# Kernel tuning notes

Hardware: AMD Instinct MI355X
Metric: run time of the kernel (lower is better)

## Reference

```python
import jax, jax.numpy as jnp
import numpy as np

EMBED_DIM = 256
NUM_HEADS = 8
NUM_QUERIES = 448
TEMPERATURE = 10000.0
SCALE = 100.0
EPS = 1e-5
B, N = 1, 512
NUM_CLASSES = 91


def box_rel_encoding(src_boxes, tgt_boxes, eps=EPS):
    # boxes: [B, N, 4] as (cx, cy, w, h)
    xy1, wh1 = src_boxes[..., :2], src_boxes[..., 2:]
    xy2, wh2 = tgt_boxes[..., :2], tgt_boxes[..., 2:]
    delta_xy = jnp.abs(xy1[..., :, None, :] - xy2[..., None, :, :])          # [B,N,N,2]
    delta_xy = jnp.log(delta_xy / (wh1[..., :, None, :] + eps) + 1.0)
    delta_wh = jnp.log((wh1[..., :, None, :] + eps) / (wh2[..., None, :, :] + eps))
    return jnp.concatenate([delta_xy, delta_wh], axis=-1)                    # [B,N,N,4]


def get_sine_pos_embed(pos, num_pos_feats, temperature=TEMPERATURE, scale=SCALE):
    # pos: [..., C]; returns [..., C * num_pos_feats]; exchange_xy=False
    dim_t = jnp.arange(num_pos_feats, dtype=pos.dtype)
    dim_t = temperature ** (2.0 * jnp.floor(dim_t / 2.0) / num_pos_feats)
    x = pos[..., None] * scale / dim_t                                        # [...,C,F]
    emb = jnp.stack([jnp.sin(x[..., 0::2]), jnp.cos(x[..., 1::2])], axis=-1)  # [...,C,F/2,2]
    emb = emb.reshape(x.shape)                                                # [...,C,F]
    return emb.reshape(pos.shape[:-1] + (pos.shape[-1] * num_pos_feats,))


def setup_inputs() -> dict:
    key = jax.random.key(0)
    ks = jax.random.split(key, 9)
    s = 0.02
    return {
        "src_boxes": jax.random.uniform(ks[0], (B, N, 4), jnp.float32, 0.05, 0.95),
        "pred_logits": jax.random.normal(ks[1], (B, N, NUM_CLASSES), jnp.float32),
        "rank_emb": jax.random.normal(ks[2], (NUM_QUERIES, EMBED_DIM), jnp.float32) * s,
        "pre_W": jax.random.normal(ks[3], (EMBED_DIM, EMBED_DIM), jnp.float32) * s,
        "pre_b": jax.random.normal(ks[4], (EMBED_DIM,), jnp.float32) * s,
        "post_W": jax.random.normal(ks[5], (EMBED_DIM, 2 * EMBED_DIM), jnp.float32) * s,
        "post_b": jax.random.normal(ks[6], (EMBED_DIM,), jnp.float32) * s,
        "attn_W": jax.random.normal(ks[7], (NUM_HEADS, EMBED_DIM), jnp.float32) * s,
        "attn_b": jax.random.normal(ks[8], (NUM_HEADS,), jnp.float32) * s,
        "layer_idx": 2,
    }


def reference(src_boxes, pred_logits, rank_emb, pre_W, pre_b, post_W, post_b, attn_W, attn_b, layer_idx):
    num_denoising = N - NUM_QUERIES
    # --- no-grad block: pairwise box relation + rank-ordered gather reorder ---
    base = box_rel_encoding(src_boxes, src_boxes)                            # [B,N,N,4]
    scores = jnp.max(jax.nn.sigmoid(pred_logits[:, num_denoising:]), axis=-1)  # [B,Q]
    order = jnp.argsort(-scores, axis=1)                                      # descending  [B,Q]
    rank_indices = jnp.broadcast_to(jnp.arange(N, dtype=order.dtype), (B, N))
    rank_indices = rank_indices.at[:, num_denoising:].set(order + num_denoising)
    nr = base[:, num_denoising:, num_denoising:]                              # [B,Q,Q,4]
    nr = jnp.take_along_axis(nr, order[:, :, None, None], axis=1)
    nr = jnp.take_along_axis(nr, order[:, None, :, None], axis=2)
    base = base.at[:, num_denoising:, num_denoising:].set(nr)
    base = jax.lax.stop_gradient(base)
    # --- sine positional embedding of relation: [B,N,N,EMBED_DIM] ---
    pos = get_sine_pos_embed(base, EMBED_DIM // 4)
    # --- rank-aware relation: embedding -> pre linear -> pairwise sum ---
    normal_rank = rank_emb @ pre_W.T + pre_b                                  # [Q,E]
    rank_rel = jnp.zeros((B, N, EMBED_DIM), src_boxes.dtype)
    rank_rel = rank_rel.at[:, num_denoising:].set(normal_rank[None])
    rank_rel = rank_rel[:, :, None, :] + rank_rel[:, None, :, :]              # [B,N,N,E]
    relation = jnp.concatenate([pos, rank_rel], axis=-1)                      # [B,N,N,2E]
    relation = relation @ post_W.T + post_b                                   # [B,N,N,E]
    attn = jax.nn.relu(relation @ attn_W.T + attn_b)                          # [B,N,N,H]
    attn = jnp.transpose(attn, (0, 3, 1, 2))                                  # [B,H,N,N]
    return attn, rank_indices
```

## Files before the change

kernel.cpp:

```cpp
#include <hip/hip_runtime.h>
#include <hip/hip_bf16.h>
#include <math.h>

#define NN 512
#define NQ 448
#define ND 64
#define NC 91
#define ED 256
#define NH 8

typedef __attribute__((ext_vector_type(8))) short bf16x8;
typedef __attribute__((ext_vector_type(4))) float f32x4;

struct FreqArg { float fr[32]; };

__device__ int   g_perm[NN];
__device__ float g_WK[2048];
__device__ float g_c0[NH];
__device__ float g_afull[NN * NH];
__device__ float g_part[64 * 512];
__device__ float g_pu[64 * ED];
__device__ float g_pb2a[64];
__device__ float g_scores[NQ];
__device__ __align__(16) unsigned short g_WB[8 * 64 * 8];

__device__ inline unsigned short f2bfbits(float x) {
    __hip_bfloat16 h = __float2bfloat16(x);
    union { __hip_bfloat16 b; unsigned short u; } cv; cv.b = h; return cv.u;
}

__global__ __launch_bounds__(512) void precomp_fold(const float* __restrict__ logits,
                                                    const float* __restrict__ attn_W,
                                                    const float* __restrict__ attn_b,
                                                    const float* __restrict__ post_W,
                                                    const float* __restrict__ post_b) {
    int bid = blockIdx.x;
    int t = threadIdx.x;
    if (bid < 64) {
        int h = bid >> 3, cc = bid & 7;
        __shared__ float sAW[32];
        if (t < 32) sAW[t] = attn_W[h * ED + cc * 32 + t];
        __syncthreads();
        float m = 0.f;
        const float* pw = post_W + (size_t)(cc * 32) * 512 + t;
#pragma unroll
        for (int ci = 0; ci < 32; ++ci) m = fmaf(sAW[ci], pw[(size_t)ci * 512], m);
        g_part[(size_t)bid * 512 + t] = m;
    } else if (bid < 72) {
        int W = (bid - 64) * 8 + (t >> 6);
        int lane = t & 63;
        for (int qi = 0; qi < 7; ++qi) {
            int q = W * 7 + qi;
            const float* row = logits + (size_t)(ND + q) * NC;
            float m = (lane < NC) ? row[lane] : -INFINITY;
            int c2 = lane + 64;
            if (c2 < NC) m = fmaxf(m, row[c2]);
            for (int off = 32; off > 0; off >>= 1) m = fmaxf(m, __shfl_down(m, off, 64));
            if (lane == 0) g_scores[q] = m;
        }
    } else {
        int h = t >> 6, lane = t & 63;
        float v = 0.f;
#pragma unroll
        for (int k = 0; k < 4; ++k) {
            int c = lane + 64 * k;
            v = fmaf(attn_W[h * ED + c], post_b[c], v);
        }
        for (int off = 32; off > 0; off >>= 1) v += __shfl_down(v, off, 64);
        if (lane == 0) g_c0[h] = attn_b[h] + v;
    }
}

__global__ __launch_bounds__(256) void precomp_u(const float* __restrict__ pre_W,
                                                 const float* __restrict__ pre_b,
                                                 float* __restrict__ out2) {
    int bid = blockIdx.x;
    int t = threadIdx.x;
    if (bid < 64) {
        int h = bid >> 3, dc = bid & 7;
        __shared__ float sw[32];
        if (t < 32) {
            int d = dc * 32 + t;
            float s = 0.f;
#pragma unroll
            for (int cc = 0; cc < 8; ++cc) s += g_part[(size_t)(h * 8 + cc) * 512 + 256 + d];
            sw[t] = s;
        } else if (t < 64) {
            int dl = t - 32;
            int d = dc * 32 + dl;
            float s = 0.f;
#pragma unroll
            for (int cc = 0; cc < 8; ++cc) s += g_part[(size_t)(h * 8 + cc) * 512 + d];
            int f = d >> 6, rem = d & 63, k = rem >> 1, r = rem & 1;
            g_WK[(k * 4 + f) * 16 + h * 2 + r] = s;
        }
        __syncthreads();
        if (t == 0) {
            float b = 0.f;
            for (int dl = 0; dl < 32; ++dl) b = fmaf(sw[dl], pre_b[dc * 32 + dl], b);
            g_pb2a[h * 8 + dc] = b;
        }
        float acc = 0.f;
        const float* pw = pre_W + (size_t)(dc * 32) * ED + t;
#pragma unroll
        for (int dl = 0; dl < 32; ++dl) acc = fmaf(sw[dl], pw[(size_t)dl * ED], acc);
        g_pu[(size_t)(h * 8 + dc) * ED + t] = acc;
    } else {
        __shared__ float sc[NQ];
        for (int v = t; v < NQ; v += 256) sc[v] = g_scores[v];
        __syncthreads();
        int q1 = t, q2 = t + 256;
        float s1 = sc[q1];
        float s2 = (q2 < NQ) ? sc[q2] : 0.f;
        int r1 = 0, r2 = 0;
        for (int j = 0; j < NQ; ++j) {
            float sj = sc[j];
            r1 += ((sj > s1) || (sj == s1 && j < q1)) ? 1 : 0;
            r2 += ((sj > s2) || (sj == s2 && j < q2)) ? 1 : 0;
        }
        g_perm[ND + r1] = ND + q1;
        out2[ND + r1] = (float)(ND + q1);
        if (q2 < NQ) {
            g_perm[ND + r2] = ND + q2;
            out2[ND + r2] = (float)(ND + q2);
        }
        if (t < ND) {
            g_perm[t] = t;
            out2[t] = (float)t;
            for (int h = 0; h < NH; ++h) g_afull[t * NH + h] = 0.f;
        }
    }
}

#define PAD 260
__global__ __launch_bounds__(256) void precomp_afull(const float* __restrict__ rank_emb) {
    int t = threadIdx.x;
    if (blockIdx.x == 14) {
        for (int v = t; v < 4096; v += 256) {
            int s = v >> 9;
            int lane = (v >> 3) & 63;
            int ii = v & 7;
            int g = lane >> 4, hh = lane & 15;
            int k = s * 4 + (ii >> 1), r = ii & 1;
            float w = (hh < NH) ? g_WK[((k * 4 + g) << 4) + hh * 2 + r] : 0.f;
            g_WB[v] = f2bfbits(w);
        }
        return;
    }
    __shared__ float sU[NH][PAD];
    __shared__ float sR[32][PAD];
    __shared__ float sb2a[NH];
    int q0 = blockIdx.x * 32;
    for (int v = t; v < NH * ED; v += 256) {
        int h = v >> 8, c = v & 255;
        float s = 0.f;
#pragma unroll
        for (int dc = 0; dc < 8; ++dc) s += g_pu[(size_t)(h * 8 + dc) * ED + c];
        sU[h][c] = s;
    }
    if (t < NH) {
        float s = 0.f;
#pragma unroll
        for (int dc = 0; dc < 8; ++dc) s += g_pb2a[t * 8 + dc];
        sb2a[t] = s;
    }
    for (int v = t; v < 32 * ED; v += 256)
        sR[v >> 8][v & 255] = rank_emb[(size_t)(q0 + (v >> 8)) * ED + (v & 255)];
    __syncthreads();
    int qloc = t >> 3, h = t & 7;
    float acc = sb2a[h];
    for (int c = 0; c < ED; ++c) acc = fmaf(sR[qloc][c], sU[h][c], acc);
    g_afull[(size_t)(ND + q0 + qloc) * NH + h] = acc;
}

__global__ __launch_bounds__(256) void relation_main(const float* __restrict__ boxes,
                                                     FreqArg fa,
                                                     float* __restrict__ out) {
    __shared__ bf16x8 sWB[8][64];
    int t = threadIdx.x;
    ((uint4*)sWB)[t]       = ((const uint4*)g_WB)[t];
    ((uint4*)sWB)[t + 256] = ((const uint4*)g_WB)[t + 256];
    __syncthreads();

    int wave = t >> 6, lane = t & 63;
    int g = lane >> 4, r = lane & 15;
    int i = blockIdx.x >> 3;
    int j = ((blockIdx.x & 7) << 6) + (wave << 4) + r;

    int pi = i, pj = j;
    if (i >= ND) { pi = g_perm[i]; if (j >= ND) pj = g_perm[j]; }
    float4 b1 = ((const float4*)boxes)[pi];
    float4 b2 = ((const float4*)boxes)[pj];
    const float eps = 1e-5f;
    float ft;
    if (g == 0)      ft = logf(fabsf(b1.x - b2.x) / (b1.z + eps) + 1.0f);
    else if (g == 1) ft = logf(fabsf(b1.y - b2.y) / (b1.w + eps) + 1.0f);
    else if (g == 2) ft = logf((b1.z + eps) / (b2.z + eps));
    else             ft = logf((b1.w + eps) / (b2.w + eps));

    f32x4 acc = {0.f, 0.f, 0.f, 0.f};
#pragma unroll
    for (int s = 0; s < 8; ++s) {
        bf16x8 bfrag;
#pragma unroll
        for (int a = 0; a < 4; ++a) {
            float rev = ft * fa.fr[s * 4 + a];
            rev -= floorf(rev);
            float sv = __builtin_amdgcn_sinf(rev);
            float cv = __builtin_amdgcn_cosf(rev);
            bfrag[2 * a]     = (short)f2bfbits(sv);
            bfrag[2 * a + 1] = (short)f2bfbits(cv);
        }
        acc = __builtin_amdgcn_mfma_f32_16x16x32_bf16(sWB[s][lane], bfrag, acc, 0, 0, 0);
    }

    if (g < 2) {
        float4 cb = *(const float4*)(g_c0 + g * 4);
        float4 ai = *(const float4*)(g_afull + i * NH + g * 4);
        float4 aj = *(const float4*)(g_afull + j * NH + g * 4);
        const float* cbp = (const float*)&cb;
        const float* aip = (const float*)&ai;
        const float* ajp = (const float*)&aj;
#pragma unroll
        for (int q = 0; q < 4; ++q) {
            int h = g * 4 + q;
            float v = acc[q] + cbp[q] + aip[q] + ajp[q];
            v = v > 0.f ? v : 0.f;
            out[(size_t)h * (NN * NN) + i * NN + j] = v;
        }
    }
}

extern "C" void kernel_launch(void* const* d_in, const int* in_sizes, int n_in,
                              void* d_out, int out_size, void* d_ws, size_t ws_size,
                              hipStream_t stream) {
    const float* boxes    = (const float*)d_in[0];
    const float* logits   = (const float*)d_in[1];
    const float* rank_emb = (const float*)d_in[2];
    const float* pre_W    = (const float*)d_in[3];
    const float* pre_b    = (const float*)d_in[4];
    const float* post_W   = (const float*)d_in[5];
    const float* post_b   = (const float*)d_in[6];
    const float* attn_W   = (const float*)d_in[7];
    const float* attn_b   = (const float*)d_in[8];
    float* out = (float*)d_out;

    precomp_fold<<<73, 512, 0, stream>>>(logits, attn_W, attn_b, post_W, post_b);
    precomp_u<<<65, 256, 0, stream>>>(pre_W, pre_b, out + (size_t)NH * NN * NN);
    precomp_afull<<<15, 256, 0, stream>>>(rank_emb);

    FreqArg fa;
    for (int k = 0; k < 32; ++k)
        fa.fr[k] = (float)(100.0 / (2.0 * M_PI) / pow(10000.0, (double)k / 32.0));

    relation_main<<<4096, 256, 0, stream>>>(boxes, fa, out);
}
```

Before: 50.43 us.

## Restructure rank precompute into two kernels and compute normal_rank directly

Three serial precompute kernels become two. The rank-embedding projection (rank_emb @ pre_W^T + pre_b) now runs in parallel blocks of the first kernel, alongside the post/attn weight fold. The second kernel then contracts the projected ranks against the folded attention weights and builds the bf16 MFMA weight table directly. This removes one launch and one dependent stage in front of the main kernel, at the cost of more precompute blocks and more shared memory. The permutation lookup also changes so that only the query-query block is permuted, which matches the reference semantics.

```diff
diff --git a/kernel.cpp b/kernel.cpp
--- a/kernel.cpp
+++ b/kernel.cpp
@@ -15,13 +15,11 @@
 struct FreqArg { float fr[32]; };
 
 __device__ int   g_perm[NN];
-__device__ float g_WK[2048];
 __device__ float g_c0[NH];
 __device__ float g_afull[NN * NH];
 __device__ float g_part[64 * 512];
-__device__ float g_pu[64 * ED];
-__device__ float g_pb2a[64];
 __device__ float g_scores[NQ];
+__device__ float g_nr[NQ * ED];
 __device__ __align__(16) unsigned short g_WB[8 * 64 * 8];
 
 __device__ inline unsigned short f2bfbits(float x) {
@@ -29,16 +27,20 @@
     union { __hip_bfloat16 b; unsigned short u; } cv; cv.b = h; return cv.u;
 }
 
-__global__ __launch_bounds__(512) void precomp_fold(const float* __restrict__ logits,
-                                                    const float* __restrict__ attn_W,
-                                                    const float* __restrict__ attn_b,
-                                                    const float* __restrict__ post_W,
-                                                    const float* __restrict__ post_b) {
+__global__ __launch_bounds__(512) void precomp1(const float* __restrict__ logits,
+                                                const float* __restrict__ attn_W,
+                                                const float* __restrict__ attn_b,
+                                                const float* __restrict__ post_W,
+                                                const float* __restrict__ post_b,
+                                                const float* __restrict__ pre_W,
+                                                const float* __restrict__ pre_b,
+                                                const float* __restrict__ rank_emb) {
+    __shared__ float smem[48 * 257];
     int bid = blockIdx.x;
     int t = threadIdx.x;
     if (bid < 64) {
         int h = bid >> 3, cc = bid & 7;
-        __shared__ float sAW[32];
+        float* sAW = smem;
         if (t < 32) sAW[t] = attn_W[h * ED + cc * 32 + t];
         __syncthreads();
         float m = 0.f;
@@ -58,7 +60,7 @@
             for (int off = 32; off > 0; off >>= 1) m = fmaxf(m, __shfl_down(m, off, 64));
             if (lane == 0) g_scores[q] = m;
         }
-    } else {
+    } else if (bid == 72) {
         int h = t >> 6, lane = t & 63;
         float v = 0.f;
 #pragma unroll
@@ -68,43 +70,68 @@
         }
         for (int off = 32; off > 0; off >>= 1) v += __shfl_down(v, off, 64);
         if (lane == 0) g_c0[h] = attn_b[h] + v;
-    }
-}
-
-__global__ __launch_bounds__(256) void precomp_u(const float* __restrict__ pre_W,
-                                                 const float* __restrict__ pre_b,
-                                                 float* __restrict__ out2) {
+    } else {
+        int nb = bid - 73;
+        int q0 = (nb >> 3) * 16, d0 = (nb & 7) * 32;
+        float* sP = smem;
+        float* sR = smem + 32 * 257;
+        for (int v = t; v < 32 * 256; v += 512)
+            sP[(v >> 8) * 257 + (v & 255)] = pre_W[(size_t)(d0 + (v >> 8)) * ED + (v & 255)];
+        for (int v = t; v < 16 * 256; v += 512)
+            sR[(v >> 8) * 257 + (v & 255)] = rank_emb[(size_t)(q0 + (v >> 8)) * ED + (v & 255)];
+        __syncthreads();
+        int q = t >> 5, dl = t & 31;
+        float acc = pre_b[d0 + dl];
+#pragma unroll 8
+        for (int e = 0; e < 256; ++e) acc = fmaf(sR[q * 257 + e], sP[dl * 257 + e], acc);
+        g_nr[(size_t)(q0 + q) * ED + d0 + dl] = acc;
+    }
+}
+
+__global__ __launch_bounds__(256) void precomp2(float* __restrict__ out2) {
     int bid = blockIdx.x;
     int t = threadIdx.x;
-    if (bid < 64) {
-        int h = bid >> 3, dc = bid & 7;
-        __shared__ float sw[32];
-        if (t < 32) {
-            int d = dc * 32 + t;
+    if (bid < 56) {
+        __shared__ float sW[NH * 260];
+        __shared__ float sN[NH * 260];
+        int q0 = bid * 8;
+        for (int v = t; v < 2048; v += 256) {
+            int h = v >> 8, d = v & 255;
             float s = 0.f;
 #pragma unroll
             for (int cc = 0; cc < 8; ++cc) s += g_part[(size_t)(h * 8 + cc) * 512 + 256 + d];
-            sw[t] = s;
-        } else if (t < 64) {
-            int dl = t - 32;
-            int d = dc * 32 + dl;
-            float s = 0.f;
-#pragma unroll
-            for (int cc = 0; cc < 8; ++cc) s += g_part[(size_t)(h * 8 + cc) * 512 + d];
-            int f = d >> 6, rem = d & 63, k = rem >> 1, r = rem & 1;
-            g_WK[(k * 4 + f) * 16 + h * 2 + r] = s;
-        }
-        __syncthreads();
-        if (t == 0) {
-            float b = 0.f;
-            for (int dl = 0; dl < 32; ++dl) b = fmaf(sw[dl], pre_b[dc * 32 + dl], b);
-            g_pb2a[h * 8 + dc] = b;
-        }
-        float acc = 0.f;
-        const float* pw = pre_W + (size_t)(dc * 32) * ED + t;
-#pragma unroll
-        for (int dl = 0; dl < 32; ++dl) acc = fmaf(sw[dl], pw[(size_t)dl * ED], acc);
-        g_pu[(size_t)(h * 8 + dc) * ED + t] = acc;
+            sW[h * 260 + d] = s;
+        }
+        for (int v = t; v < 2048; v += 256)
+            sN[(v >> 8) * 260 + (v & 255)] = g_nr[(size_t)(q0 + (v >> 8)) * ED + (v & 255)];
+        __syncthreads();
+        int o = t >> 2, sub = t & 3;
+        int q = o >> 3, h = o & 7;
+        float a = 0.f;
+#pragma unroll 8
+        for (int e2 = 0; e2 < 64; ++e2) {
+            int e = sub + 4 * e2;
+            a = fmaf(sN[q * 260 + e], sW[h * 260 + e], a);
+        }
+        a += __shfl_xor(a, 1, 64);
+        a += __shfl_xor(a, 2, 64);
+        if (sub == 0) g_afull[(size_t)(ND + q0 + q) * NH + h] = a;
+    } else if (bid < 58) {
+        for (int vv = t; vv < 2048; vv += 256) {
+            int v = (bid - 56) * 2048 + vv;
+            int s = v >> 9;
+            int lane = (v >> 3) & 63;
+            int ii = v & 7;
+            int g = lane >> 4, hh = lane & 15;
+            int k = s * 4 + (ii >> 1), r = ii & 1;
+            int d = g * 64 + 2 * k + r;
+            float w = 0.f;
+            if (hh < NH) {
+#pragma unroll
+                for (int cc = 0; cc < 8; ++cc) w += g_part[(size_t)(hh * 8 + cc) * 512 + d];
+            }
+            g_WB[v] = f2bfbits(w);
+        }
     } else {
         __shared__ float sc[NQ];
         for (int v = t; v < NQ; v += 256) sc[v] = g_scores[v];
@@ -132,47 +159,6 @@
     }
 }
 
-#define PAD 260
-__global__ __launch_bounds__(256) void precomp_afull(const float* __restrict__ rank_emb) {
-    int t = threadIdx.x;
-    if (blockIdx.x == 14) {
-        for (int v = t; v < 4096; v += 256) {
-            int s = v >> 9;
-            int lane = (v >> 3) & 63;
-            int ii = v & 7;
-            int g = lane >> 4, hh = lane & 15;
-            int k = s * 4 + (ii >> 1), r = ii & 1;
-            float w = (hh < NH) ? g_WK[((k * 4 + g) << 4) + hh * 2 + r] : 0.f;
-            g_WB[v] = f2bfbits(w);
-        }
-        return;
-    }
-    __shared__ float sU[NH][PAD];
-    __shared__ float sR[32][PAD];
-    __shared__ float sb2a[NH];
-    int q0 = blockIdx.x * 32;
-    for (int v = t; v < NH * ED; v += 256) {
-        int h = v >> 8, c = v & 255;
-        float s = 0.f;
-#pragma unroll
-        for (int dc = 0; dc < 8; ++dc) s += g_pu[(size_t)(h * 8 + dc) * ED + c];
-        sU[h][c] = s;
-    }
-    if (t < NH) {
-        float s = 0.f;
-#pragma unroll
-        for (int dc = 0; dc < 8; ++dc) s += g_pb2a[t * 8 + dc];
-        sb2a[t] = s;
-    }
-    for (int v = t; v < 32 * ED; v += 256)
-        sR[v >> 8][v & 255] = rank_emb[(size_t)(q0 + (v >> 8)) * ED + (v & 255)];
-    __syncthreads();
-    int qloc = t >> 3, h = t & 7;
-    float acc = sb2a[h];
-    for (int c = 0; c < ED; ++c) acc = fmaf(sR[qloc][c], sU[h][c], acc);
-    g_afull[(size_t)(ND + q0 + qloc) * NH + h] = acc;
-}
-
 __global__ __launch_bounds__(256) void relation_main(const float* __restrict__ boxes,
                                                      FreqArg fa,
                                                      float* __restrict__ out) {
@@ -188,7 +174,7 @@
     int j = ((blockIdx.x & 7) << 6) + (wave << 4) + r;
 
     int pi = i, pj = j;
-    if (i >= ND) { pi = g_perm[i]; if (j >= ND) pj = g_perm[j]; }
+    if (i >= ND && j >= ND) { pi = g_perm[i]; pj = g_perm[j]; }
     float4 b1 = ((const float4*)boxes)[pi];
     float4 b2 = ((const float4*)boxes)[pj];
     const float eps = 1e-5f;
@@ -245,9 +231,9 @@
     const float* attn_b   = (const float*)d_in[8];
     float* out = (float*)d_out;
 
-    precomp_fold<<<73, 512, 0, stream>>>(logits, attn_W, attn_b, post_W, post_b);
-    precomp_u<<<65, 256, 0, stream>>>(pre_W, pre_b, out + (size_t)NH * NN * NN);
-    precomp_afull<<<15, 256, 0, stream>>>(rank_emb);
+    precomp1<<<297, 512, 0, stream>>>(logits, attn_W, attn_b, post_W, post_b,
+                                      pre_W, pre_b, rank_emb);
+    precomp2<<<59, 256, 0, stream>>>(out + (size_t)NH * NN * NN);
 
     FreqArg fa;
     for (int k = 0; k < 32; ++k)
```

Result: faster. 45.02 us (-10.7%).
